# Kernel tuning notes

Hardware: AMD Instinct MI355X
Metric: run time of the kernel (lower is better)

Reference implementation:

```python
import jax, jax.numpy as jnp
import numpy as np


def setup_inputs() -> dict:
    key = jax.random.key(0)
    k1, k2 = jax.random.split(key)
    B, C, H, W = 8, 128, 192, 256
    a = jax.random.normal(k1, (B, C, H, W), dtype=jnp.float32)
    b = jax.random.normal(k2, (B, C, H, W), dtype=jnp.float32)
    return {"a": a, "b": b, "max_displacement": 40}


def reference(a, b, max_displacement):
    """Horizontal correlation cost volume.

    out[:, ctr, h, w] = sum_c a[:, c, h, w] * b[:, c, h, w - (D - ctr)]
    for ctr in 0..D (out-of-range b treated as zero), matching the torch
    shift-and-pad loop over displacements i = -D..0.
    """
    D = max_displacement
    W = a.shape[-1]
    # Pad b once on the left by D; then the shifted slice for index ctr is
    # bp[..., ctr:ctr+W]  (static slices -> jit-friendly, no big stack kept).
    bp = jnp.pad(b, ((0, 0), (0, 0), (0, 0), (D, 0)))
    outs = [jnp.einsum('bchw,bchw->bhw', a, bp[..., ctr:ctr + W])
            for ctr in range(D + 1)]  # small fixed loop over D+1 displacements
    return jnp.stack(outs, axis=1)  # [B, D+1, H, W]
```

## Files before the change

### kernel.cpp

```cpp
#include <hip/hip_runtime.h>


constexpr int Bsz = 8, Cch = 128, Hh = 192, Ww = 256, NC = 41;
constexpr int CHW = Hh * Ww;
constexpr int LDB = 40;
constexpr int A_BYTES = 256 * LDB * 2;
constexpr int OSTRIDE = 260;

using sh4 = __attribute__((ext_vector_type(4))) short;
using sh8 = __attribute__((ext_vector_type(8))) short;
using fx4 = __attribute__((ext_vector_type(4))) float;

__device__ inline unsigned short f2bf(float x) {
    unsigned int u = __float_as_uint(x);
    u += 0x7fffu + ((u >> 16) & 1u);
    return (unsigned short)(u >> 16);
}

__global__ __launch_bounds__(512, 4)
void corr_mfma(const float* __restrict__ A, const float* __restrict__ B,
               float* __restrict__ O) {
    __shared__ __align__(16) unsigned char smem[44800];
    unsigned short* aT   = (unsigned short*)smem;
    unsigned short* bT   = (unsigned short*)(smem + A_BYTES);
    float*          outp = (float*)smem;

    const int tid  = threadIdx.x;
    const int lane = tid & 63, wave = tid >> 6;
    const int row  = blockIdx.x;
    const int bb   = row / Hh, h = row - bb * Hh;

    const float* base_a = A + (size_t)bb * Cch * CHW + (size_t)h * Ww;
    const float* base_b = B + (size_t)bb * Cch * CHW + (size_t)h * Ww;

    const int cg = tid & 7;
    const int w4 = tid >> 3;
    const int wi = lane & 15, kg = lane >> 4;

    const float* pa0 = base_a + (size_t)(cg * 4) * CHW + w4 * 4;
    const float* pb0 = base_b + (size_t)(cg * 4) * CHW + w4 * 4;

    fx4 acc[2][4];
#pragma unroll
    for (int i = 0; i < 2; ++i)
#pragma unroll
        for (int j = 0; j < 4; ++j) acc[i][j] = (fx4)0.0f;

    float4 rA[2][4], rB[2][4];

#define ISSUE(S, K)                                                           \
    _Pragma("unroll")                                                         \
    for (int i = 0; i < 4; ++i)                                               \
        rA[S][i] = *(const float4*)(pa0 + (size_t)((K) * 32 + i) * CHW);      \
    _Pragma("unroll")                                                         \
    for (int i = 0; i < 4; ++i)                                               \
        rB[S][i] = *(const float4*)(pb0 + (size_t)((K) * 32 + i) * CHW);

#define CONV_STORE(S)                                                         \
    {                                                                         \
        const float* fa = (const float*)&rA[S][0];                            \
        const float* fb = (const float*)&rB[S][0];                            \
        _Pragma("unroll")                                                     \
        for (int r = 0; r < 4; ++r) {                                         \
            sh4 s;                                                            \
            _Pragma("unroll")                                                 \
            for (int i = 0; i < 4; ++i) s[i] = (short)f2bf(fa[i * 4 + r]);    \
            *(sh4*)(aT + (w4 * 4 + r) * LDB + cg * 4) = s;                    \
        }                                                                     \
        _Pragma("unroll")                                                     \
        for (int r = 0; r < 4; ++r) {                                         \
            sh4 s;                                                            \
            _Pragma("unroll")                                                 \
            for (int i = 0; i < 4; ++i) s[i] = (short)f2bf(fb[i * 4 + r]);    \
            *(sh4*)(bT + (40 + w4 * 4 + r) * LDB + cg * 4) = s;               \
        }                                                                     \
    }

#define MFMA_STEP()                                                           \
    {                                                                         \
        const int w0 = wave * 32;                                             \
        sh8 afr[2], bfr[5];                                                   \
        _Pragma("unroll")                                                     \
        for (int i = 0; i < 2; ++i)                                           \
            afr[i] = *(const sh8*)(aT + (w0 + i * 16 + wi) * LDB + kg * 8);   \
        _Pragma("unroll")                                                     \
        for (int t = 0; t < 5; ++t)                                           \
            bfr[t] = *(const sh8*)(bT + (w0 + t * 16 + wi) * LDB + kg * 8);   \
        _Pragma("unroll")                                                     \
        for (int i = 0; i < 2; ++i)                                           \
            _Pragma("unroll")                                                 \
            for (int j = 0; j < 4; ++j)                                       \
                acc[i][j] = __builtin_amdgcn_mfma_f32_16x16x32_bf16(          \
                    bfr[i + j], afr[i], acc[i][j], 0, 0, 0);                  \
    }

#define DS_BAR()                                           \
    asm volatile("s_waitcnt lgkmcnt(0)" ::: "memory");     \
    __builtin_amdgcn_s_barrier();                          \
    asm volatile("" ::: "memory");

    ISSUE(0, 0)
    if (tid < 320) {
        int u = tid >> 3, cz = (tid & 7) * 4;
        *(sh4*)(bT + u * LDB + cz) = (sh4)0;
    }
    ISSUE(1, 1)
    CONV_STORE(0)
    ISSUE(0, 2)
    DS_BAR()
    MFMA_STEP()
    DS_BAR()
    CONV_STORE(1)
    ISSUE(1, 3)
    DS_BAR()
    MFMA_STEP()
    DS_BAR()
    CONV_STORE(0)
    DS_BAR()
    MFMA_STEP()
    DS_BAR()
    CONV_STORE(1)
    DS_BAR()
    MFMA_STEP()

    DS_BAR()
#pragma unroll
    for (int i = 0; i < 2; ++i) {
        const int w0 = wave * 32 + i * 16;
#pragma unroll
        for (int j = 0; j < 4; ++j)
#pragma unroll
            for (int r = 0; r < 4; ++r) {
                int ctr = 16 * j + (kg * 4 + r) - wi;
                if ((unsigned)ctr <= 40u) outp[ctr * OSTRIDE + w0 + wi] = acc[i][j][r];
            }
    }
    DS_BAR()
    float* obase = O + ((size_t)bb * NC * Hh + (size_t)h) * Ww;
    for (int idx = tid; idx < NC * 64; idx += 512) {
        int ctr = idx >> 6, q = idx & 63;
        float4 v = *(const float4*)(outp + ctr * OSTRIDE + q * 4);
        *(float4*)(obase + (size_t)ctr * CHW + q * 4) = v;
    }
}

extern "C" void kernel_launch(void* const* d_in, const int* in_sizes, int n_in,
                              void* d_out, int out_size, void* d_ws, size_t ws_size,
                              hipStream_t stream) {
    const float* a = (const float*)d_in[0];
    const float* b = (const float*)d_in[1];
    float* out = (float*)d_out;
    corr_mfma<<<dim3(Bsz * Hh), dim3(512), 0, stream>>>(a, b, out);
}
```

Before: 408.0 us.

## Process three rows per block with a continuous cross-row load/compute pipeline

```diff
diff --git a/kernel.cpp b/kernel.cpp
--- a/kernel.cpp
+++ b/kernel.cpp
@@ -6,6 +6,8 @@
 constexpr int LDB = 40;
 constexpr int A_BYTES = 256 * LDB * 2;
 constexpr int OSTRIDE = 260;
+constexpr int RPB = 3;
+constexpr int NCHUNK = 4 * RPB;
 
 using sh4 = __attribute__((ext_vector_type(4))) short;
 using sh8 = __attribute__((ext_vector_type(8))) short;
@@ -27,11 +29,11 @@
 
     const int tid  = threadIdx.x;
     const int lane = tid & 63, wave = tid >> 6;
-    const int row  = blockIdx.x;
-    const int bb   = row / Hh, h = row - bb * Hh;
+    const int row0 = blockIdx.x * RPB;
+    const int bb   = row0 / Hh, h0 = row0 - bb * Hh;
 
-    const float* base_a = A + (size_t)bb * Cch * CHW + (size_t)h * Ww;
-    const float* base_b = B + (size_t)bb * Cch * CHW + (size_t)h * Ww;
+    const float* base_a = A + (size_t)bb * Cch * CHW + (size_t)h0 * Ww;
+    const float* base_b = B + (size_t)bb * Cch * CHW + (size_t)h0 * Ww;
 
     const int cg = tid & 7;
     const int w4 = tid >> 3;
@@ -46,20 +48,22 @@
 #pragma unroll
         for (int j = 0; j < 4; ++j) acc[i][j] = (fx4)0.0f;
 
-    float4 rA[2][4], rB[2][4];
+    float4 rA[4], rB[4];
 
-#define ISSUE(S, K)                                                           \
+#define ISSUE(G)                                                              \
     _Pragma("unroll")                                                         \
     for (int i = 0; i < 4; ++i)                                               \
-        rA[S][i] = *(const float4*)(pa0 + (size_t)((K) * 32 + i) * CHW);      \
+        rA[i] = *(const float4*)(pa0 + (size_t)(((G) >> 2) * Ww) +            \
+                                 (size_t)(((G) & 3) * 32 + i) * CHW);         \
     _Pragma("unroll")                                                         \
     for (int i = 0; i < 4; ++i)                                               \
-        rB[S][i] = *(const float4*)(pb0 + (size_t)((K) * 32 + i) * CHW);
+        rB[i] = *(const float4*)(pb0 + (size_t)(((G) >> 2) * Ww) +            \
+                                 (size_t)(((G) & 3) * 32 + i) * CHW);
 
-#define CONV_STORE(S)                                                         \
+#define CONV_STORE()                                                          \
     {                                                                         \
-        const float* fa = (const float*)&rA[S][0];                            \
-        const float* fb = (const float*)&rB[S][0];                            \
+        const float* fa = (const float*)&rA[0];                               \
+        const float* fb = (const float*)&rB[0];                               \
         _Pragma("unroll")                                                     \
         for (int r = 0; r < 4; ++r) {                                         \
             sh4 s;                                                            \
@@ -99,48 +103,57 @@
     __builtin_amdgcn_s_barrier();                          \
     asm volatile("" ::: "memory");
 
-    ISSUE(0, 0)
-    if (tid < 320) {
-        int u = tid >> 3, cz = (tid & 7) * 4;
-        *(sh4*)(bT + u * LDB + cz) = (sh4)0;
+#define REZERO()                                           \
+    if (tid < 320) {                                       \
+        int u = tid >> 3, cz = (tid & 7) * 4;              \
+        *(sh4*)(bT + u * LDB + cz) = (sh4)0;               \
     }
-    ISSUE(1, 1)
-    CONV_STORE(0)
-    ISSUE(0, 2)
-    DS_BAR()
-    MFMA_STEP()
-    DS_BAR()
-    CONV_STORE(1)
-    ISSUE(1, 3)
-    DS_BAR()
-    MFMA_STEP()
-    DS_BAR()
-    CONV_STORE(0)
-    DS_BAR()
-    MFMA_STEP()
-    DS_BAR()
-    CONV_STORE(1)
-    DS_BAR()
-    MFMA_STEP()
 
-    DS_BAR()
+    ISSUE(0)
+    __builtin_amdgcn_sched_barrier(0);
+    REZERO()
+
 #pragma unroll
-    for (int i = 0; i < 2; ++i) {
-        const int w0 = wave * 32 + i * 16;
+    for (int g = 0; g < NCHUNK; ++g) {
+        const int k = g & 3;
+        CONV_STORE()
+        if (k == 0 && g > 0) { REZERO() }
+        if (g + 1 < NCHUNK) { ISSUE(g + 1) }
+        __builtin_amdgcn_sched_barrier(0);
+        DS_BAR()
+        MFMA_STEP()
+        DS_BAR()
+        if (k == 3) {
+            const int r = g >> 2;
 #pragma unroll
-        for (int j = 0; j < 4; ++j)
+            for (int i = 0; i < 2; ++i) {
+                const int w0 = wave * 32 + i * 16;
 #pragma unroll
-            for (int r = 0; r < 4; ++r) {
-                int ctr = 16 * j + (kg * 4 + r) - wi;
-                if ((unsigned)ctr <= 40u) outp[ctr * OSTRIDE + w0 + wi] = acc[i][j][r];
+                for (int j = 0; j < 4; ++j)
+#pragma unroll
+                    for (int rr = 0; rr < 4; ++rr) {
+                        int ctr = 16 * j + (kg * 4 + rr) - wi;
+                        if ((unsigned)ctr <= 40u)
+                            outp[ctr * OSTRIDE + w0 + wi] = acc[i][j][rr];
+                    }
             }
-    }
-    DS_BAR()
-    float* obase = O + ((size_t)bb * NC * Hh + (size_t)h) * Ww;
-    for (int idx = tid; idx < NC * 64; idx += 512) {
-        int ctr = idx >> 6, q = idx & 63;
-        float4 v = *(const float4*)(outp + ctr * OSTRIDE + q * 4);
-        *(float4*)(obase + (size_t)ctr * CHW + q * 4) = v;
+            DS_BAR()
+            float* obase = O + ((size_t)bb * NC * Hh + (size_t)(h0 + r)) * Ww;
+#pragma unroll
+            for (int ii = 0; ii < 6; ++ii) {
+                int idx = tid + ii * 512;
+                if (idx < NC * 64) {
+                    int ctr = idx >> 6, q = idx & 63;
+                    float4 v = *(const float4*)(outp + ctr * OSTRIDE + q * 4);
+                    *(float4*)(obase + (size_t)ctr * CHW + q * 4) = v;
+                }
+            }
+            DS_BAR()
+#pragma unroll
+            for (int i = 0; i < 2; ++i)
+#pragma unroll
+                for (int j = 0; j < 4; ++j) acc[i][j] = (fx4)0.0f;
+        }
     }
 }
 
@@ -150,5 +163,5 @@
     const float* a = (const float*)d_in[0];
     const float* b = (const float*)d_in[1];
     float* out = (float*)d_out;
-    corr_mfma<<<dim3(Bsz * Hh), dim3(512), 0, stream>>>(a, b, out);
+    corr_mfma<<<dim3(Bsz * Hh / RPB), dim3(512), 0, stream>>>(a, b, out);
 }
```

Measured after the change: 414.5 us. Within noise of the previous version (+1.6%).

## Stage inputs via global_load_lds double-buffer with fine-grained convert pipeline

Applied to the files above, without the earlier changes.

```diff
diff --git a/kernel.cpp b/kernel.cpp
--- a/kernel.cpp
+++ b/kernel.cpp
@@ -5,6 +5,9 @@
 constexpr int CHW = Hh * Ww;
 constexpr int LDB = 40;
 constexpr int A_BYTES = 256 * LDB * 2;
+constexpr int B_BYTES = 304 * LDB * 2;
+constexpr int STAGE_OFF = A_BYTES + B_BYTES;
+constexpr int SMEM_BYTES = STAGE_OFF + 2 * 8192;
 constexpr int OSTRIDE = 260;
 
 using sh4 = __attribute__((ext_vector_type(4))) short;
@@ -17,12 +20,20 @@
     return (unsigned short)(u >> 16);
 }
 
+typedef const __attribute__((address_space(1))) void gv_t;
+typedef __attribute__((address_space(3))) void lv_t;
+#define GLL(g, l) __builtin_amdgcn_global_load_lds((gv_t*)(g), (lv_t*)(l), 16, 0, 0)
+#define VMWAIT(N) asm volatile("s_waitcnt vmcnt(" #N ")" ::: "memory")
+#define LGKM0()   asm volatile("s_waitcnt lgkmcnt(0)" ::: "memory")
+#define BAR()     __builtin_amdgcn_s_barrier()
+
 __global__ __launch_bounds__(512, 4)
 void corr_mfma(const float* __restrict__ A, const float* __restrict__ B,
                float* __restrict__ O) {
-    __shared__ __align__(16) unsigned char smem[44800];
+    __shared__ __align__(16) unsigned char smem[SMEM_BYTES];
     unsigned short* aT   = (unsigned short*)smem;
     unsigned short* bT   = (unsigned short*)(smem + A_BYTES);
+    float*          stg  = (float*)(smem + STAGE_OFF);
     float*          outp = (float*)smem;
 
     const int tid  = threadIdx.x;
@@ -30,15 +41,16 @@
     const int row  = blockIdx.x;
     const int bb   = row / Hh, h = row - bb * Hh;
 
-    const float* base_a = A + (size_t)bb * Cch * CHW + (size_t)h * Ww;
-    const float* base_b = B + (size_t)bb * Cch * CHW + (size_t)h * Ww;
+    const float* gsrc0 = ((wave < 4) ? A : B)
+                       + (size_t)bb * Cch * CHW + (size_t)h * Ww
+                       + (size_t)(wave & 3) * CHW + lane * 4;
+    float* ldst0 = stg + wave * 256;
 
-    const int cg = tid & 7;
-    const int w4 = tid >> 3;
+    const int tt = tid >> 8, wcol = tid & 255;
+    const float* cstg = stg + tt * 1024 + wcol;
+    unsigned short* tdst = tt ? (bT + (40 + wcol) * LDB) : (aT + wcol * LDB);
+
     const int wi = lane & 15, kg = lane >> 4;
-
-    const float* pa0 = base_a + (size_t)(cg * 4) * CHW + w4 * 4;
-    const float* pb0 = base_b + (size_t)(cg * 4) * CHW + w4 * 4;
 
     fx4 acc[2][4];
 #pragma unroll
@@ -46,34 +58,16 @@
 #pragma unroll
         for (int j = 0; j < 4; ++j) acc[i][j] = (fx4)0.0f;
 
-    float4 rA[2][4], rB[2][4];
+#define GISSUE(S) GLL(gsrc0 + (size_t)(S) * 4 * CHW, ldst0 + ((S) & 1) * 2048)
 
-#define ISSUE(S, K)                                                           \
-    _Pragma("unroll")                                                         \
-    for (int i = 0; i < 4; ++i)                                               \
-        rA[S][i] = *(const float4*)(pa0 + (size_t)((K) * 32 + i) * CHW);      \
-    _Pragma("unroll")                                                         \
-    for (int i = 0; i < 4; ++i)                                               \
-        rB[S][i] = *(const float4*)(pb0 + (size_t)((K) * 32 + i) * CHW);
-
-#define CONV_STORE(S)                                                         \
+#define CONVERT(S)                                                            \
     {                                                                         \
-        const float* fa = (const float*)&rA[S][0];                            \
-        const float* fb = (const float*)&rB[S][0];                            \
-        _Pragma("unroll")                                                     \
-        for (int r = 0; r < 4; ++r) {                                         \
-            sh4 s;                                                            \
-            _Pragma("unroll")                                                 \
-            for (int i = 0; i < 4; ++i) s[i] = (short)f2bf(fa[i * 4 + r]);    \
-            *(sh4*)(aT + (w4 * 4 + r) * LDB + cg * 4) = s;                    \
-        }                                                                     \
-        _Pragma("unroll")                                                     \
-        for (int r = 0; r < 4; ++r) {                                         \
-            sh4 s;                                                            \
-            _Pragma("unroll")                                                 \
-            for (int i = 0; i < 4; ++i) s[i] = (short)f2bf(fb[i * 4 + r]);    \
-            *(sh4*)(bT + (40 + w4 * 4 + r) * LDB + cg * 4) = s;               \
-        }                                                                     \
+        const float* sp = cstg + ((S) & 1) * 2048;                            \
+        float f0 = sp[0], f1 = sp[256], f2 = sp[512], f3 = sp[768];           \
+        sh4 v;                                                                \
+        v[0] = (short)f2bf(f0); v[1] = (short)f2bf(f1);                       \
+        v[2] = (short)f2bf(f2); v[3] = (short)f2bf(f3);                       \
+        *(sh4*)(tdst + ((S) & 7) * 4) = v;                                    \
     }
 
 #define MFMA_STEP()                                                           \
@@ -94,53 +88,56 @@
                     bfr[i + j], afr[i], acc[i][j], 0, 0, 0);                  \
     }
 
-#define DS_BAR()                                           \
-    asm volatile("s_waitcnt lgkmcnt(0)" ::: "memory");     \
-    __builtin_amdgcn_s_barrier();                          \
-    asm volatile("" ::: "memory");
-
-    ISSUE(0, 0)
+    GISSUE(0);
+    GISSUE(1);
     if (tid < 320) {
         int u = tid >> 3, cz = (tid & 7) * 4;
         *(sh4*)(bT + u * LDB + cz) = (sh4)0;
+    } else if (tid < 384) {
+        int x = tid - 320;
+        int u = 296 + (x >> 3), cz = (x & 7) * 4;
+        *(sh4*)(bT + u * LDB + cz) = (sh4)0;
     }
-    ISSUE(1, 1)
-    CONV_STORE(0)
-    ISSUE(0, 2)
-    DS_BAR()
-    MFMA_STEP()
-    DS_BAR()
-    CONV_STORE(1)
-    ISSUE(1, 3)
-    DS_BAR()
-    MFMA_STEP()
-    DS_BAR()
-    CONV_STORE(0)
-    DS_BAR()
-    MFMA_STEP()
-    DS_BAR()
-    CONV_STORE(1)
-    DS_BAR()
-    MFMA_STEP()
 
-    DS_BAR()
+#pragma unroll
+    for (int k = 0; k < 4; ++k) {
+#pragma unroll
+        for (int j = 0; j < 8; ++j) {
+            const int s = k * 8 + j;
+            if (s < 31) { VMWAIT(1); } else { VMWAIT(0); }
+            BAR();
+            CONVERT(s)
+            LGKM0();
+            BAR();
+            if (s + 2 < 32) { GISSUE(s + 2); }
+        }
+        MFMA_STEP()
+    }
+
+    LGKM0();
+    BAR();
 #pragma unroll
     for (int i = 0; i < 2; ++i) {
         const int w0 = wave * 32 + i * 16;
 #pragma unroll
         for (int j = 0; j < 4; ++j)
 #pragma unroll
-            for (int r = 0; r < 4; ++r) {
-                int ctr = 16 * j + (kg * 4 + r) - wi;
-                if ((unsigned)ctr <= 40u) outp[ctr * OSTRIDE + w0 + wi] = acc[i][j][r];
+            for (int rr = 0; rr < 4; ++rr) {
+                int ctr = 16 * j + (kg * 4 + rr) - wi;
+                if ((unsigned)ctr <= 40u) outp[ctr * OSTRIDE + w0 + wi] = acc[i][j][rr];
             }
     }
-    DS_BAR()
+    LGKM0();
+    BAR();
     float* obase = O + ((size_t)bb * NC * Hh + (size_t)h) * Ww;
-    for (int idx = tid; idx < NC * 64; idx += 512) {
-        int ctr = idx >> 6, q = idx & 63;
-        float4 v = *(const float4*)(outp + ctr * OSTRIDE + q * 4);
-        *(float4*)(obase + (size_t)ctr * CHW + q * 4) = v;
+#pragma unroll
+    for (int ii = 0; ii < 6; ++ii) {
+        int idx = tid + ii * 512;
+        if (idx < NC * 64) {
+            int ctr = idx >> 6, q = idx & 63;
+            float4 v = *(const float4*)(outp + ctr * OSTRIDE + q * 4);
+            *(float4*)(obase + (size_t)ctr * CHW + q * 4) = v;
+        }
     }
 }
 
```

Result: no change. 405.0 us (-0.7%).
